# Kernel optimization log

Measured on AMD Instinct MI355X. Metric: run time of the kernel, lower is better.

## Reference

```python
import jax, jax.numpy as jnp
import numpy as np


def _quat_to_rot(q):
    # q: (N,4) wxyz -> (N,3,3)
    q = q / jnp.linalg.norm(q, axis=1, keepdims=True)
    w, x, y, z = q[:, 0], q[:, 1], q[:, 2], q[:, 3]
    R = jnp.stack([
        1 - 2 * y * y - 2 * z * z, 2 * x * y - 2 * w * z, 2 * x * z + 2 * w * y,
        2 * x * y + 2 * w * z, 1 - 2 * x * x - 2 * z * z, 2 * y * z - 2 * w * x,
        2 * x * z - 2 * w * y, 2 * y * z + 2 * w * x, 1 - 2 * x * x - 2 * y * y,
    ], axis=1)
    return R.reshape(-1, 3, 3)


def _forward(camera_poses, positions, scales, rotations, opacity, features, H, W):
    B = camera_poses.shape[0]
    N = positions.shape[0]
    # --- project positions: hom @ pose^T ---
    hom = jnp.concatenate([positions, jnp.ones((N, 1), positions.dtype)], axis=1)  # (N,4)
    cam = jnp.einsum('ni,bji->bnj', hom, camera_poses)  # (B,N,4)
    depths = cam[..., 2]                                 # (B,N)
    pos2d = cam[..., :2] / depths[..., None]             # (B,N,2)
    # --- 3D covariance: R S S R^T ---
    R = _quat_to_rot(rotations)                          # (N,3,3)
    cov3d = jnp.einsum('nik,nk,njk->nij', R, scales * scales, R)  # (N,3,3)
    # --- perspective Jacobian (original uses world-space z, kept faithful) ---
    fx = camera_poses[:, 0, 0][:, None]  # (B,1)
    fy = camera_poses[:, 1, 1][:, None]
    z = positions[:, 2][None, :]         # (1,N)
    zero = jnp.zeros_like(fx * z)        # (B,N)
    row0 = jnp.stack([fx / z, zero, -fx * positions[None, :, 0] / (z * z)], axis=-1)
    row1 = jnp.stack([zero, fy / z, -fy * positions[None, :, 1] / (z * z)], axis=-1)
    J = jnp.stack([row0, row1], axis=-2)                 # (B,N,2,3)
    cov2d = jnp.einsum('bnij,njk,bnlk->bnil', J, cov3d, J)  # (B,N,2,2)
    # --- back-to-front order (descending depth) ---
    order = jnp.argsort(-depths, axis=1)                 # (B,N)
    pos_s = jnp.take_along_axis(pos2d, order[..., None], axis=1)
    cov_s = jnp.take_along_axis(cov2d, order[..., None, None], axis=1)
    color_s = features[order]                            # (B,N,3)
    alpha_s = opacity[order, 0]                          # (B,N)
    # analytic 2x2 inverse
    a = cov_s[..., 0, 0]; b = cov_s[..., 0, 1]; c = cov_s[..., 1, 0]; d = cov_s[..., 1, 1]
    det = a * d - b * c
    inv = jnp.stack([jnp.stack([d, -b], -1), jnp.stack([-c, a], -1)], -2) / det[..., None, None]
    # pixel grid in [-1,1], (H,W,2) with x first (matches torch stack([x,y]))
    ys = jnp.linspace(-1.0, 1.0, H)
    xs = jnp.linspace(-1.0, 1.0, W)
    yy, xx = jnp.meshgrid(ys, xs, indexing='ij')
    grid = jnp.stack([xx, yy], axis=-1)
    # --- splat + alpha compositing (sequential loop expressed as exclusive cumprod) ---
    diff = grid[None, None] - pos_s[:, :, None, None, :]           # (B,N,H,W,2)
    maha = jnp.einsum('bnhwi,bnij,bnhwj->bnhw', diff, inv, diff)   # (B,N,H,W)
    alpha_map = jnp.exp(-0.5 * maha) * alpha_s[:, :, None, None]   # (B,N,H,W)
    trans = jnp.cumprod(1.0 - alpha_map, axis=1)
    T = jnp.concatenate([jnp.ones_like(trans[:, :1]), trans[:, :-1]], axis=1)  # exclusive
    weight = T * alpha_map
    return jnp.einsum('bnhw,bnc->bchw', weight, color_s)          # (B,3,H,W)


def setup_inputs() -> dict:
    key = jax.random.key(0)
    ks = jax.random.split(key, 6)
    N, B = 2048, 1
    positions = jax.random.uniform(ks[0], (N, 3), minval=-1.0, maxval=1.0)
    scales = jax.random.uniform(ks[1], (N, 3), minval=0.001, maxval=0.1)
    rot = jnp.concatenate([jnp.ones((N, 1)), 0.01 * jax.random.normal(ks[2], (N, 3))], axis=1)
    rotations = rot / jnp.linalg.norm(rot, axis=1, keepdims=True)
    opacity = jax.random.uniform(ks[3], (N, 1), minval=0.0, maxval=0.02)
    features = jax.random.uniform(ks[4], (N, 3))
    pose = jnp.eye(4) + 0.01 * jax.random.normal(ks[5], (4, 4))
    pose = pose.at[2, 3].add(3.0).at[3].set(jnp.array([0.0, 0.0, 0.0, 1.0]))
    camera_poses = jnp.broadcast_to(pose, (B, 4, 4))
    return {"camera_poses": camera_poses, "positions": positions, "scales": scales,
            "rotations": rotations, "opacity": opacity, "features": features,
            "H": 96, "W": 96}


def reference(camera_poses, positions, scales, rotations, opacity, features, H, W):
    return _forward(camera_poses, positions, scales, rotations, opacity, features, H, W)
```

## Files before the change

kernel.cpp:

```cpp
#include <hip/hip_runtime.h>
#include <math.h>

#define TPB 256
#define PIXPT 4
#define NSEG_MAX 64

__device__ __forceinline__ unsigned int f2ord(float f) {
    unsigned int u = __float_as_uint(f);
    return (u & 0x80000000u) ? ~u : (u | 0x80000000u);
}

__global__ void gs_prep_rank(const float* __restrict__ pose,
                             const float* __restrict__ positions,
                             const float* __restrict__ scales,
                             const float* __restrict__ rotations,
                             const float* __restrict__ opacity,
                             const float* __restrict__ features,
                             float* __restrict__ sorted,
                             int N)
{
    extern __shared__ unsigned long long skey[];
    const int b = blockIdx.y;
    const float* P = pose + b * 16;
    const float C_EXP = -0.72134752044448170f;

    for (int n = threadIdx.x; n < N; n += TPB) {
        float x = positions[n * 3 + 0];
        float y = positions[n * 3 + 1];
        float z = positions[n * 3 + 2];
        float depth = P[8] * x + P[9] * y + P[10] * z + P[11];
        skey[n] = ((unsigned long long)(~f2ord(depth)) << 32) | (unsigned int)n;
    }
    __syncthreads();

    int g = blockIdx.x * 32 + (threadIdx.x >> 3);
    int s = threadIdx.x & 7;
    if (g >= N) return;
    unsigned long long kn = skey[g];
    int cnt = 0;
    for (int m = s; m < N; m += 8) cnt += (skey[m] < kn) ? 1 : 0;
    cnt += __shfl_down(cnt, 4, 8);
    cnt += __shfl_down(cnt, 2, 8);
    cnt += __shfl_down(cnt, 1, 8);
    if (s != 0) return;
    int rank = cnt;

    float x = positions[g * 3 + 0];
    float y = positions[g * 3 + 1];
    float z = positions[g * 3 + 2];

    float depth = P[8] * x + P[9] * y + P[10] * z + P[11];
    float inv_d = 1.0f / depth;
    float mx = (P[0] * x + P[1] * y + P[2] * z + P[3]) * inv_d;
    float my = (P[4] * x + P[5] * y + P[6] * z + P[7]) * inv_d;

    float qw = rotations[g * 4 + 0];
    float qx = rotations[g * 4 + 1];
    float qy = rotations[g * 4 + 2];
    float qz = rotations[g * 4 + 3];
    float qn = sqrtf(qw * qw + qx * qx + qy * qy + qz * qz);
    qw /= qn; qx /= qn; qy /= qn; qz /= qn;
    float R00 = 1.f - 2.f * (qy * qy + qz * qz);
    float R01 = 2.f * (qx * qy - qw * qz);
    float R02 = 2.f * (qx * qz + qw * qy);
    float R10 = 2.f * (qx * qy + qw * qz);
    float R11 = 1.f - 2.f * (qx * qx + qz * qz);
    float R12 = 2.f * (qy * qz - qw * qx);
    float R20 = 2.f * (qx * qz - qw * qy);
    float R21 = 2.f * (qy * qz + qw * qx);
    float R22 = 1.f - 2.f * (qx * qx + qy * qy);

    float s0 = scales[g * 3 + 0];
    float s1 = scales[g * 3 + 1];
    float s2 = scales[g * 3 + 2];
    float v0 = s0 * s0, v1 = s1 * s1, v2 = s2 * s2;

    float C00 = R00 * R00 * v0 + R01 * R01 * v1 + R02 * R02 * v2;
    float C01 = R00 * R10 * v0 + R01 * R11 * v1 + R02 * R12 * v2;
    float C02 = R00 * R20 * v0 + R01 * R21 * v1 + R02 * R22 * v2;
    float C11 = R10 * R10 * v0 + R11 * R11 * v1 + R12 * R12 * v2;
    float C12 = R10 * R20 * v0 + R11 * R21 * v1 + R12 * R22 * v2;
    float C22 = R20 * R20 * v0 + R21 * R21 * v1 + R22 * R22 * v2;

    float fx = P[0], fy = P[5];
    float iz = 1.0f / z;
    float a0 = fx * iz;
    float c0 = -fx * x * iz * iz;
    float b1 = fy * iz;
    float c1 = -fy * y * iz * iz;

    float cov00 = a0 * a0 * C00 + 2.f * a0 * c0 * C02 + c0 * c0 * C22;
    float cov01 = a0 * b1 * C01 + a0 * c1 * C02 + c0 * b1 * C12 + c0 * c1 * C22;
    float cov11 = b1 * b1 * C11 + 2.f * b1 * c1 * C12 + c1 * c1 * C22;

    float det = cov00 * cov11 - cov01 * cov01;
    float invdet = 1.0f / det;
    float A  = C_EXP * cov11 * invdet;
    float Bc = C_EXP * -2.0f * cov01 * invdet;
    float D  = C_EXP * cov00 * invdet;
    float l2a = log2f(opacity[g]);

    float4* p4 = (float4*)(sorted + ((size_t)b * N + rank) * 12);
    p4[0] = make_float4(mx, my, A, Bc);
    p4[1] = make_float4(D, l2a, features[g * 3 + 0], features[g * 3 + 1]);
    p4[2] = make_float4(features[g * 3 + 2], 0.f, 0.f, 0.f);
}

__global__ void gs_raster_partial(const float* __restrict__ sorted,
                                  float* __restrict__ partials,
                                  const int* __restrict__ pH,
                                  const int* __restrict__ pW,
                                  int N, int B, int HW, int nseg)
{
    extern __shared__ float4 sg4[];
    int H = *pH;
    int W = *pW;
    int seg = blockIdx.y;
    int seglen = (N + nseg - 1) / nseg;
    int g0 = seg * seglen;
    int g1 = g0 + seglen; if (g1 > N) g1 = N;
    int cnt = g1 - g0; if (cnt < 0) cnt = 0;

    int pixbase = blockIdx.x * (TPB * PIXPT);
    int b = pixbase / HW;

    const float4* src = (const float4*)(sorted + ((size_t)b * N + g0) * 12);
    for (int i = threadIdx.x; i < cnt * 3; i += TPB) sg4[i] = src[i];
    __syncthreads();

    float px[PIXPT], py[PIXPT];
    float T[PIXPT], cr[PIXPT], cg[PIXPT], cb[PIXPT];
    bool valid[PIXPT];
    #pragma unroll
    for (int k = 0; k < PIXPT; ++k) {
        int pix = pixbase + threadIdx.x + k * TPB;
        valid[k] = (pix < B * HW);
        int pp = valid[k] ? (pix - b * HW) : 0;
        int h = pp / W;
        int w = pp - h * W;
        px[k] = 2.0f * (float)w / (float)(W - 1) - 1.0f;
        py[k] = 2.0f * (float)h / (float)(H - 1) - 1.0f;
        T[k] = 1.0f; cr[k] = 0.f; cg[k] = 0.f; cb[k] = 0.f;
    }

    for (int g = 0; g < cnt; ++g) {
        float4 f0 = sg4[g * 3 + 0];
        float4 f1 = sg4[g * 3 + 1];
        float4 f2 = sg4[g * 3 + 2];
        #pragma unroll
        for (int k = 0; k < PIXPT; ++k) {
            float dx = px[k] - f0.x;
            float dy = py[k] - f0.y;
            float q = f1.y;
            q = fmaf(f1.x * dy, dy, q);
            q = fmaf(f0.w * dx, dy, q);
            q = fmaf(f0.z * dx, dx, q);
            float am = exp2f(q);
            float wgt = T[k] * am;
            cr[k] = fmaf(wgt, f1.z, cr[k]);
            cg[k] = fmaf(wgt, f1.w, cg[k]);
            cb[k] = fmaf(wgt, f2.x, cb[k]);
            T[k] = fmaf(-am, T[k], T[k]);
        }
    }

    #pragma unroll
    for (int k = 0; k < PIXPT; ++k) {
        int pix = pixbase + threadIdx.x + k * TPB;
        if (!valid[k]) continue;
        float4* o = (float4*)(partials + ((size_t)seg * (size_t)(B * HW) + pix) * 4);
        *o = make_float4(cr[k], cg[k], cb[k], T[k]);
    }
}

__global__ void gs_combine(const float* __restrict__ partials,
                           float* __restrict__ out,
                           int B, int HW, int nseg)
{
    int pix = blockIdx.x * blockDim.x + threadIdx.x;
    if (pix >= B * HW) return;
    int b = pix / HW;
    int pp = pix - b * HW;
    float T = 1.0f, cr = 0.f, cg = 0.f, cb = 0.f;
    for (int s = 0; s < nseg; ++s) {
        float4 p = *(const float4*)(partials + ((size_t)s * (size_t)(B * HW) + pix) * 4);
        cr = fmaf(T, p.x, cr);
        cg = fmaf(T, p.y, cg);
        cb = fmaf(T, p.z, cb);
        T *= p.w;
    }
    out[((size_t)b * 3 + 0) * HW + pp] = cr;
    out[((size_t)b * 3 + 1) * HW + pp] = cg;
    out[((size_t)b * 3 + 2) * HW + pp] = cb;
}

extern "C" void kernel_launch(void* const* d_in, const int* in_sizes, int n_in,
                              void* d_out, int out_size, void* d_ws, size_t ws_size,
                              hipStream_t stream)
{
    const float* pose      = (const float*)d_in[0];
    const float* positions = (const float*)d_in[1];
    const float* scales    = (const float*)d_in[2];
    const float* rotations = (const float*)d_in[3];
    const float* opacity   = (const float*)d_in[4];
    const float* features  = (const float*)d_in[5];
    const int*   pH        = (const int*)d_in[6];
    const int*   pW        = (const int*)d_in[7];

    int B = in_sizes[0] / 16;
    int N = in_sizes[1] / 3;
    int HW = out_size / (3 * B);

    float* out = (float*)d_out;

    char* wp = (char*)d_ws;
    float* sorted = (float*)wp;
    wp += ((size_t)B * N * 12 * sizeof(float) + 15) & ~(size_t)15;
    float* partials = (float*)wp;

    size_t used = (size_t)(wp - (char*)d_ws);
    size_t avail = ws_size > used ? ws_size - used : 0;
    long long ns = (long long)(avail / ((size_t)B * HW * 4 * sizeof(float)));
    int nseg = (int)(ns > NSEG_MAX ? NSEG_MAX : ns);
    if (nseg < 1) nseg = 1;

    dim3 g1((N + 31) / 32, B);
    gs_prep_rank<<<g1, TPB, N * sizeof(unsigned long long), stream>>>(
        pose, positions, scales, rotations, opacity, features, sorted, N);

    int seglen = (N + nseg - 1) / nseg;
    dim3 g3((B * HW + TPB * PIXPT - 1) / (TPB * PIXPT), nseg);
    gs_raster_partial<<<g3, TPB, (size_t)seglen * 3 * sizeof(float4), stream>>>(
        sorted, partials, pH, pW, N, B, HW, nseg);

    gs_combine<<<(B * HW + TPB - 1) / TPB, TPB, 0, stream>>>(
        partials, out, B, HW, nseg);
}
```

Baseline: 120.9 us.

## Fuse prep, raster and combine into one persistent kernel with flag barriers

Merges the three launches (depth rank plus projection, segmented rasterization, segment combine) into a single persistent kernel. The blocks stride over prep jobs, raster jobs and combine jobs and meet at software grid barriers built from per-block flags in workspace. The goal is to remove the launch gaps and tail drain between kernels. The segment count is now set from a block cap instead of the workspace size. The flags are never reset between calls, so on repeat calls the barriers may pass immediately and phases can race. The scheme also relies on every block being resident at the same time, or it deadlocks.

```diff
diff --git a/kernel.cpp b/kernel.cpp
--- a/kernel.cpp
+++ b/kernel.cpp
@@ -4,194 +4,229 @@
 #define TPB 256
 #define PIXPT 4
 #define NSEG_MAX 64
+#define MAXBLOCKS 1024
+#define MAGIC1 0x13579BDFu
+#define MAGIC2 0x2468ACE1u
 
 __device__ __forceinline__ unsigned int f2ord(float f) {
     unsigned int u = __float_as_uint(f);
     return (u & 0x80000000u) ? ~u : (u | 0x80000000u);
 }
 
-__global__ void gs_prep_rank(const float* __restrict__ pose,
-                             const float* __restrict__ positions,
-                             const float* __restrict__ scales,
-                             const float* __restrict__ rotations,
-                             const float* __restrict__ opacity,
-                             const float* __restrict__ features,
-                             float* __restrict__ sorted,
-                             int N)
+__device__ __forceinline__ void flag_barrier(unsigned int* flags, int nblocks,
+                                             unsigned int magic)
 {
-    extern __shared__ unsigned long long skey[];
-    const int b = blockIdx.y;
-    const float* P = pose + b * 16;
+    __syncthreads();
+    if (threadIdx.x == 0) {
+        __hip_atomic_store(&flags[blockIdx.x], magic,
+                           __ATOMIC_RELEASE, __HIP_MEMORY_SCOPE_AGENT);
+    }
+    for (int i = threadIdx.x; i < nblocks; i += TPB) {
+        while (__hip_atomic_load(&flags[i], __ATOMIC_ACQUIRE,
+                                 __HIP_MEMORY_SCOPE_AGENT) != magic) {
+            __builtin_amdgcn_s_sleep(2);
+        }
+    }
+    __syncthreads();
+}
+
+extern __shared__ char smem[];
+
+__global__ __launch_bounds__(TPB, 4) void gs_fused(
+    const float* __restrict__ pose,
+    const float* __restrict__ positions,
+    const float* __restrict__ scales,
+    const float* __restrict__ rotations,
+    const float* __restrict__ opacity,
+    const float* __restrict__ features,
+    const int* __restrict__ pH,
+    const int* __restrict__ pW,
+    unsigned int* __restrict__ flagsA,
+    unsigned int* __restrict__ flagsB,
+    float* __restrict__ sorted,
+    float* __restrict__ partials,
+    float* __restrict__ out,
+    int N, int B, int HW, int PB, int nseg, int nblocks)
+{
     const float C_EXP = -0.72134752044448170f;
-
-    for (int n = threadIdx.x; n < N; n += TPB) {
-        float x = positions[n * 3 + 0];
-        float y = positions[n * 3 + 1];
-        float z = positions[n * 3 + 2];
-        float depth = P[8] * x + P[9] * y + P[10] * z + P[11];
-        skey[n] = ((unsigned long long)(~f2ord(depth)) << 32) | (unsigned int)n;
-    }
-    __syncthreads();
-
-    int g = blockIdx.x * 32 + (threadIdx.x >> 3);
-    int s = threadIdx.x & 7;
-    if (g >= N) return;
-    unsigned long long kn = skey[g];
-    int cnt = 0;
-    for (int m = s; m < N; m += 8) cnt += (skey[m] < kn) ? 1 : 0;
-    cnt += __shfl_down(cnt, 4, 8);
-    cnt += __shfl_down(cnt, 2, 8);
-    cnt += __shfl_down(cnt, 1, 8);
-    if (s != 0) return;
-    int rank = cnt;
-
-    float x = positions[g * 3 + 0];
-    float y = positions[g * 3 + 1];
-    float z = positions[g * 3 + 2];
-
-    float depth = P[8] * x + P[9] * y + P[10] * z + P[11];
-    float inv_d = 1.0f / depth;
-    float mx = (P[0] * x + P[1] * y + P[2] * z + P[3]) * inv_d;
-    float my = (P[4] * x + P[5] * y + P[6] * z + P[7]) * inv_d;
-
-    float qw = rotations[g * 4 + 0];
-    float qx = rotations[g * 4 + 1];
-    float qy = rotations[g * 4 + 2];
-    float qz = rotations[g * 4 + 3];
-    float qn = sqrtf(qw * qw + qx * qx + qy * qy + qz * qz);
-    qw /= qn; qx /= qn; qy /= qn; qz /= qn;
-    float R00 = 1.f - 2.f * (qy * qy + qz * qz);
-    float R01 = 2.f * (qx * qy - qw * qz);
-    float R02 = 2.f * (qx * qz + qw * qy);
-    float R10 = 2.f * (qx * qy + qw * qz);
-    float R11 = 1.f - 2.f * (qx * qx + qz * qz);
-    float R12 = 2.f * (qy * qz - qw * qx);
-    float R20 = 2.f * (qx * qz - qw * qy);
-    float R21 = 2.f * (qy * qz + qw * qx);
-    float R22 = 1.f - 2.f * (qx * qx + qy * qy);
-
-    float s0 = scales[g * 3 + 0];
-    float s1 = scales[g * 3 + 1];
-    float s2 = scales[g * 3 + 2];
-    float v0 = s0 * s0, v1 = s1 * s1, v2 = s2 * s2;
-
-    float C00 = R00 * R00 * v0 + R01 * R01 * v1 + R02 * R02 * v2;
-    float C01 = R00 * R10 * v0 + R01 * R11 * v1 + R02 * R12 * v2;
-    float C02 = R00 * R20 * v0 + R01 * R21 * v1 + R02 * R22 * v2;
-    float C11 = R10 * R10 * v0 + R11 * R11 * v1 + R12 * R12 * v2;
-    float C12 = R10 * R20 * v0 + R11 * R21 * v1 + R12 * R22 * v2;
-    float C22 = R20 * R20 * v0 + R21 * R21 * v1 + R22 * R22 * v2;
-
-    float fx = P[0], fy = P[5];
-    float iz = 1.0f / z;
-    float a0 = fx * iz;
-    float c0 = -fx * x * iz * iz;
-    float b1 = fy * iz;
-    float c1 = -fy * y * iz * iz;
-
-    float cov00 = a0 * a0 * C00 + 2.f * a0 * c0 * C02 + c0 * c0 * C22;
-    float cov01 = a0 * b1 * C01 + a0 * c1 * C02 + c0 * b1 * C12 + c0 * c1 * C22;
-    float cov11 = b1 * b1 * C11 + 2.f * b1 * c1 * C12 + c1 * c1 * C22;
-
-    float det = cov00 * cov11 - cov01 * cov01;
-    float invdet = 1.0f / det;
-    float A  = C_EXP * cov11 * invdet;
-    float Bc = C_EXP * -2.0f * cov01 * invdet;
-    float D  = C_EXP * cov00 * invdet;
-    float l2a = log2f(opacity[g]);
-
-    float4* p4 = (float4*)(sorted + ((size_t)b * N + rank) * 12);
-    p4[0] = make_float4(mx, my, A, Bc);
-    p4[1] = make_float4(D, l2a, features[g * 3 + 0], features[g * 3 + 1]);
-    p4[2] = make_float4(features[g * 3 + 2], 0.f, 0.f, 0.f);
-}
-
-__global__ void gs_raster_partial(const float* __restrict__ sorted,
-                                  float* __restrict__ partials,
-                                  const int* __restrict__ pH,
-                                  const int* __restrict__ pW,
-                                  int N, int B, int HW, int nseg)
-{
-    extern __shared__ float4 sg4[];
-    int H = *pH;
-    int W = *pW;
-    int seg = blockIdx.y;
+    const int H = *pH;
+    const int W = *pW;
+
+    int nprep = (N + 31) >> 5;
+    for (int job = blockIdx.x; job < B * nprep; job += nblocks) {
+        int b  = job / nprep;
+        int cb = job - b * nprep;
+        const float* P = pose + b * 16;
+        unsigned long long* skey = (unsigned long long*)smem;
+
+        for (int n = threadIdx.x; n < N; n += TPB) {
+            float x = positions[n * 3 + 0];
+            float y = positions[n * 3 + 1];
+            float z = positions[n * 3 + 2];
+            float depth = P[8] * x + P[9] * y + P[10] * z + P[11];
+            skey[n] = ((unsigned long long)(~f2ord(depth)) << 32) | (unsigned int)n;
+        }
+        __syncthreads();
+
+        int g = cb * 32 + (threadIdx.x >> 3);
+        int s = threadIdx.x & 7;
+        if (g < N) {
+            unsigned long long kn = skey[g];
+            int cnt = 0;
+            for (int m = s; m < N; m += 8) cnt += (skey[m] < kn) ? 1 : 0;
+            cnt += __shfl_down(cnt, 4, 8);
+            cnt += __shfl_down(cnt, 2, 8);
+            cnt += __shfl_down(cnt, 1, 8);
+            if (s == 0) {
+                int rank = cnt;
+                float x = positions[g * 3 + 0];
+                float y = positions[g * 3 + 1];
+                float z = positions[g * 3 + 2];
+
+                float depth = P[8] * x + P[9] * y + P[10] * z + P[11];
+                float inv_d = 1.0f / depth;
+                float mx = (P[0] * x + P[1] * y + P[2] * z + P[3]) * inv_d;
+                float my = (P[4] * x + P[5] * y + P[6] * z + P[7]) * inv_d;
+
+                float qw = rotations[g * 4 + 0];
+                float qx = rotations[g * 4 + 1];
+                float qy = rotations[g * 4 + 2];
+                float qz = rotations[g * 4 + 3];
+                float qn = sqrtf(qw * qw + qx * qx + qy * qy + qz * qz);
+                qw /= qn; qx /= qn; qy /= qn; qz /= qn;
+                float R00 = 1.f - 2.f * (qy * qy + qz * qz);
+                float R01 = 2.f * (qx * qy - qw * qz);
+                float R02 = 2.f * (qx * qz + qw * qy);
+                float R10 = 2.f * (qx * qy + qw * qz);
+                float R11 = 1.f - 2.f * (qx * qx + qz * qz);
+                float R12 = 2.f * (qy * qz - qw * qx);
+                float R20 = 2.f * (qx * qz - qw * qy);
+                float R21 = 2.f * (qy * qz + qw * qx);
+                float R22 = 1.f - 2.f * (qx * qx + qy * qy);
+
+                float s0 = scales[g * 3 + 0];
+                float s1 = scales[g * 3 + 1];
+                float s2 = scales[g * 3 + 2];
+                float v0 = s0 * s0, v1 = s1 * s1, v2 = s2 * s2;
+
+                float C00 = R00 * R00 * v0 + R01 * R01 * v1 + R02 * R02 * v2;
+                float C01 = R00 * R10 * v0 + R01 * R11 * v1 + R02 * R12 * v2;
+                float C02 = R00 * R20 * v0 + R01 * R21 * v1 + R02 * R22 * v2;
+                float C11 = R10 * R10 * v0 + R11 * R11 * v1 + R12 * R12 * v2;
+                float C12 = R10 * R20 * v0 + R11 * R21 * v1 + R12 * R22 * v2;
+                float C22 = R20 * R20 * v0 + R21 * R21 * v1 + R22 * R22 * v2;
+
+                float fx = P[0], fy = P[5];
+                float iz = 1.0f / z;
+                float a0 = fx * iz;
+                float c0 = -fx * x * iz * iz;
+                float b1 = fy * iz;
+                float c1 = -fy * y * iz * iz;
+
+                float cov00 = a0 * a0 * C00 + 2.f * a0 * c0 * C02 + c0 * c0 * C22;
+                float cov01 = a0 * b1 * C01 + a0 * c1 * C02 + c0 * b1 * C12 + c0 * c1 * C22;
+                float cov11 = b1 * b1 * C11 + 2.f * b1 * c1 * C12 + c1 * c1 * C22;
+
+                float det = cov00 * cov11 - cov01 * cov01;
+                float invdet = 1.0f / det;
+                float A  = C_EXP * cov11 * invdet;
+                float Bc = C_EXP * -2.0f * cov01 * invdet;
+                float D  = C_EXP * cov00 * invdet;
+                float l2a = log2f(opacity[g]);
+
+                float4* p4 = (float4*)(sorted + ((size_t)b * N + rank) * 12);
+                p4[0] = make_float4(mx, my, A, Bc);
+                p4[1] = make_float4(D, l2a, features[g * 3 + 0], features[g * 3 + 1]);
+                p4[2] = make_float4(features[g * 3 + 2], 0.f, 0.f, 0.f);
+            }
+        }
+        __syncthreads();
+    }
+
+    flag_barrier(flagsA, nblocks, MAGIC1);
+
     int seglen = (N + nseg - 1) / nseg;
-    int g0 = seg * seglen;
-    int g1 = g0 + seglen; if (g1 > N) g1 = N;
-    int cnt = g1 - g0; if (cnt < 0) cnt = 0;
-
-    int pixbase = blockIdx.x * (TPB * PIXPT);
-    int b = pixbase / HW;
-
-    const float4* src = (const float4*)(sorted + ((size_t)b * N + g0) * 12);
-    for (int i = threadIdx.x; i < cnt * 3; i += TPB) sg4[i] = src[i];
-    __syncthreads();
-
-    float px[PIXPT], py[PIXPT];
-    float T[PIXPT], cr[PIXPT], cg[PIXPT], cb[PIXPT];
-    bool valid[PIXPT];
-    #pragma unroll
-    for (int k = 0; k < PIXPT; ++k) {
-        int pix = pixbase + threadIdx.x + k * TPB;
-        valid[k] = (pix < B * HW);
-        int pp = valid[k] ? (pix - b * HW) : 0;
-        int h = pp / W;
-        int w = pp - h * W;
-        px[k] = 2.0f * (float)w / (float)(W - 1) - 1.0f;
-        py[k] = 2.0f * (float)h / (float)(H - 1) - 1.0f;
-        T[k] = 1.0f; cr[k] = 0.f; cg[k] = 0.f; cb[k] = 0.f;
-    }
-
-    for (int g = 0; g < cnt; ++g) {
-        float4 f0 = sg4[g * 3 + 0];
-        float4 f1 = sg4[g * 3 + 1];
-        float4 f2 = sg4[g * 3 + 2];
+    for (int job = blockIdx.x; job < PB * nseg; job += nblocks) {
+        int pb  = job % PB;
+        int seg = job / PB;
+        int g0 = seg * seglen;
+        int g1 = g0 + seglen; if (g1 > N) g1 = N;
+        int cnt = g1 - g0; if (cnt < 0) cnt = 0;
+
+        int pixbase = pb * (TPB * PIXPT);
+        int b = pixbase / HW;
+
+        float4* sg4 = (float4*)smem;
+        const float4* src = (const float4*)(sorted + ((size_t)b * N + g0) * 12);
+        for (int i = threadIdx.x; i < cnt * 3; i += TPB) sg4[i] = src[i];
+        __syncthreads();
+
+        float px[PIXPT], py[PIXPT];
+        float T[PIXPT], cr[PIXPT], cg[PIXPT], cb2[PIXPT];
+        bool valid[PIXPT];
         #pragma unroll
         for (int k = 0; k < PIXPT; ++k) {
-            float dx = px[k] - f0.x;
-            float dy = py[k] - f0.y;
-            float q = f1.y;
-            q = fmaf(f1.x * dy, dy, q);
-            q = fmaf(f0.w * dx, dy, q);
-            q = fmaf(f0.z * dx, dx, q);
-            float am = exp2f(q);
-            float wgt = T[k] * am;
-            cr[k] = fmaf(wgt, f1.z, cr[k]);
-            cg[k] = fmaf(wgt, f1.w, cg[k]);
-            cb[k] = fmaf(wgt, f2.x, cb[k]);
-            T[k] = fmaf(-am, T[k], T[k]);
-        }
-    }
-
-    #pragma unroll
-    for (int k = 0; k < PIXPT; ++k) {
-        int pix = pixbase + threadIdx.x + k * TPB;
-        if (!valid[k]) continue;
-        float4* o = (float4*)(partials + ((size_t)seg * (size_t)(B * HW) + pix) * 4);
-        *o = make_float4(cr[k], cg[k], cb[k], T[k]);
-    }
-}
-
-__global__ void gs_combine(const float* __restrict__ partials,
-                           float* __restrict__ out,
-                           int B, int HW, int nseg)
-{
-    int pix = blockIdx.x * blockDim.x + threadIdx.x;
-    if (pix >= B * HW) return;
-    int b = pix / HW;
-    int pp = pix - b * HW;
-    float T = 1.0f, cr = 0.f, cg = 0.f, cb = 0.f;
-    for (int s = 0; s < nseg; ++s) {
-        float4 p = *(const float4*)(partials + ((size_t)s * (size_t)(B * HW) + pix) * 4);
-        cr = fmaf(T, p.x, cr);
-        cg = fmaf(T, p.y, cg);
-        cb = fmaf(T, p.z, cb);
-        T *= p.w;
-    }
-    out[((size_t)b * 3 + 0) * HW + pp] = cr;
-    out[((size_t)b * 3 + 1) * HW + pp] = cg;
-    out[((size_t)b * 3 + 2) * HW + pp] = cb;
+            int pix = pixbase + threadIdx.x + k * TPB;
+            valid[k] = (pix < B * HW);
+            int pp = valid[k] ? (pix - b * HW) : 0;
+            int h = pp / W;
+            int w = pp - h * W;
+            px[k] = 2.0f * (float)w / (float)(W - 1) - 1.0f;
+            py[k] = 2.0f * (float)h / (float)(H - 1) - 1.0f;
+            T[k] = 1.0f; cr[k] = 0.f; cg[k] = 0.f; cb2[k] = 0.f;
+        }
+
+        for (int g = 0; g < cnt; ++g) {
+            float4 f0 = sg4[g * 3 + 0];
+            float4 f1 = sg4[g * 3 + 1];
+            float4 f2 = sg4[g * 3 + 2];
+            #pragma unroll
+            for (int k = 0; k < PIXPT; ++k) {
+                float dx = px[k] - f0.x;
+                float dy = py[k] - f0.y;
+                float q = f1.y;
+                q = fmaf(f1.x * dy, dy, q);
+                q = fmaf(f0.w * dx, dy, q);
+                q = fmaf(f0.z * dx, dx, q);
+                float am = exp2f(q);
+                float wgt = T[k] * am;
+                cr[k]  = fmaf(wgt, f1.z, cr[k]);
+                cg[k]  = fmaf(wgt, f1.w, cg[k]);
+                cb2[k] = fmaf(wgt, f2.x, cb2[k]);
+                T[k] = fmaf(-am, T[k], T[k]);
+            }
+        }
+
+        #pragma unroll
+        for (int k = 0; k < PIXPT; ++k) {
+            int pix = pixbase + threadIdx.x + k * TPB;
+            if (!valid[k]) continue;
+            float4* o = (float4*)(partials + ((size_t)seg * (size_t)(B * HW) + pix) * 4);
+            *o = make_float4(cr[k], cg[k], cb2[k], T[k]);
+        }
+        __syncthreads();
+    }
+
+    flag_barrier(flagsB, nblocks, MAGIC2);
+
+    int ncomb = (B * HW + TPB - 1) / TPB;
+    for (int job = blockIdx.x; job < ncomb; job += nblocks) {
+        int pix = job * TPB + threadIdx.x;
+        if (pix >= B * HW) continue;
+        int b = pix / HW;
+        int pp = pix - b * HW;
+        float T = 1.0f, cr = 0.f, cg = 0.f, cb2 = 0.f;
+        for (int s = 0; s < nseg; ++s) {
+            float4 p = *(const float4*)(partials + ((size_t)s * (size_t)(B * HW) + pix) * 4);
+            cr  = fmaf(T, p.x, cr);
+            cg  = fmaf(T, p.y, cg);
+            cb2 = fmaf(T, p.z, cb2);
+            T *= p.w;
+        }
+        out[((size_t)b * 3 + 0) * HW + pp] = cr;
+        out[((size_t)b * 3 + 1) * HW + pp] = cg;
+        out[((size_t)b * 3 + 2) * HW + pp] = cb2;
+    }
 }
 
 extern "C" void kernel_launch(void* const* d_in, const int* in_sizes, int n_in,
@@ -213,26 +248,30 @@
 
     float* out = (float*)d_out;
 
+    int PB = (B * HW + TPB * PIXPT - 1) / (TPB * PIXPT);
+    int nseg = NSEG_MAX;
+    while (PB * nseg > MAXBLOCKS && nseg > 1) nseg >>= 1;
+    int nblocks = PB * nseg;
+    int nprep = (N + 31) >> 5;
+    if (nblocks < B * nprep) nblocks = B * nprep;
+    if (nblocks > MAXBLOCKS) nblocks = MAXBLOCKS;
+
     char* wp = (char*)d_ws;
+    unsigned int* flagsA = (unsigned int*)wp;
+    wp += ((size_t)nblocks * sizeof(unsigned int) + 15) & ~(size_t)15;
+    unsigned int* flagsB = (unsigned int*)wp;
+    wp += ((size_t)nblocks * sizeof(unsigned int) + 15) & ~(size_t)15;
     float* sorted = (float*)wp;
     wp += ((size_t)B * N * 12 * sizeof(float) + 15) & ~(size_t)15;
     float* partials = (float*)wp;
 
-    size_t used = (size_t)(wp - (char*)d_ws);
-    size_t avail = ws_size > used ? ws_size - used : 0;
-    long long ns = (long long)(avail / ((size_t)B * HW * 4 * sizeof(float)));
-    int nseg = (int)(ns > NSEG_MAX ? NSEG_MAX : ns);
-    if (nseg < 1) nseg = 1;
-
-    dim3 g1((N + 31) / 32, B);
-    gs_prep_rank<<<g1, TPB, N * sizeof(unsigned long long), stream>>>(
-        pose, positions, scales, rotations, opacity, features, sorted, N);
-
     int seglen = (N + nseg - 1) / nseg;
-    dim3 g3((B * HW + TPB * PIXPT - 1) / (TPB * PIXPT), nseg);
-    gs_raster_partial<<<g3, TPB, (size_t)seglen * 3 * sizeof(float4), stream>>>(
-        sorted, partials, pH, pW, N, B, HW, nseg);
-
-    gs_combine<<<(B * HW + TPB - 1) / TPB, TPB, 0, stream>>>(
-        partials, out, B, HW, nseg);
-}
+    size_t smem_a = (size_t)N * sizeof(unsigned long long);
+    size_t smem_b = (size_t)seglen * 3 * sizeof(float4);
+    size_t smem = smem_a > smem_b ? smem_a : smem_b;
+
+    gs_fused<<<nblocks, TPB, smem, stream>>>(
+        pose, positions, scales, rotations, opacity, features, pH, pW,
+        flagsA, flagsB, sorted, partials, out,
+        N, B, HW, PB, nseg, nblocks);
+}
```

After: 278.8 us. 131% more time.
